# Kernel tuning notes

Measured on AMD Instinct MI355X. Metric: run time of the kernel, lower is better.

The kernel has to match this reference:

```python
import jax, jax.numpy as jnp
import numpy as np

N_NODES = 10000
N_EDGES = 320000
D = 256


def setup_inputs() -> dict:
    key = jax.random.key(0)
    k_x, k_w, k_m, k_s, k_d = jax.random.split(key, 5)
    x = jax.random.normal(k_x, (N_NODES, D), dtype=jnp.float32)
    W = jax.random.normal(k_w, (D, D), dtype=jnp.float32)
    M = jax.random.normal(k_m, (D, D), dtype=jnp.float32)
    edge_src = jax.random.randint(k_s, (N_EDGES,), 0, N_NODES, dtype=jnp.int64)
    edge_dst = jax.random.randint(k_d, (N_EDGES,), 0, N_NODES, dtype=jnp.int64)
    return {"x": x, "W": W, "M": M, "edge_src": edge_src, "edge_dst": edge_dst}


def reference(x, W, M, edge_src, edge_dst):
    # Synchronous GCN-style update: new_x_i = relu(x_i @ W + sum_{j in N(i)} x_j @ M)
    # Transform once [N,d]@[d,d], then gather per-edge and segment-sum into destinations.
    self_term = x @ W                      # [N, d]
    msg = x @ M                            # [N, d]
    agg = jax.ops.segment_sum(msg[edge_src], edge_dst, num_segments=x.shape[0])  # [N, d]
    return jax.nn.relu(self_term + agg)
```

## Files before the change

kernel.cpp:

```cpp
#include <hip/hip_runtime.h>
#include <hip/hip_bf16.h>
#include <stdint.h>

#define N_NODES 10000
#define N_EDGES 320000
#define DD 256
#define BKT 96

typedef __attribute__((ext_vector_type(4))) float f32x4;
typedef __attribute__((ext_vector_type(8))) short short8;
typedef __attribute__((ext_vector_type(4))) short short4v;

__device__ __forceinline__ short f2b(float f) {
  unsigned u = __builtin_bit_cast(unsigned, f);
  u += 0x7fffu + ((u >> 16) & 1u);
  return (short)(u >> 16);
}
__device__ __forceinline__ float b2f(short s) {
  return __builtin_bit_cast(float, ((unsigned)(unsigned short)s) << 16);
}

__global__ __launch_bounds__(256) void k_pre(const float* __restrict__ x,
                                             const float* __restrict__ W,
                                             const float* __restrict__ M,
                                             const int* __restrict__ esrc,
                                             const int* __restrict__ edst,
                                             short* __restrict__ xb,
                                             short* __restrict__ Bb,
                                             int* __restrict__ cnt,
                                             int* __restrict__ srcs) {
  const int b = blockIdx.x, t = threadIdx.x;
  if (b < 2500) {
    int i = (b * 256 + t) * 4;
    f32x4 v = *(const f32x4*)(x + i);
    short4v o;
    o[0] = f2b(v[0]); o[1] = f2b(v[1]); o[2] = f2b(v[2]); o[3] = f2b(v[3]);
    *(short4v*)(xb + i) = o;
  } else if (b < 2756) {
    int n = b - 2500;
    Bb[n * 512 + t]       = f2b(W[t * DD + n]);
    Bb[n * 512 + t + 256] = f2b(M[t * DD + n]);
  } else {
    int e = (b - 2756) * 256 + t;
    int d = edst[e];
    int pos = atomicAdd(&cnt[d], 1);
    if (pos < BKT) srcs[d * BKT + pos] = esrc[e];
  }
}

__global__ __launch_bounds__(256) void k_agg(const short* __restrict__ xb,
                                             const int* __restrict__ cnt,
                                             const int* __restrict__ srcs,
                                             short* __restrict__ axb) {
  const int wave = threadIdx.x >> 6, lane = threadIdx.x & 63;
  const int node = blockIdx.x * 4 + wave;
  const int col = lane * 4;
  const int* bkt = srcs + node * BKT;
  float a0 = 0.f, a1 = 0.f, a2 = 0.f, a3 = 0.f;
  const int d = cnt[node];
  int e = 0;
  for (; e + 16 <= d; e += 16) {
    int sidx[16];
    #pragma unroll
    for (int q = 0; q < 16; q++) sidx[q] = bkt[e + q];
    short4v vv[16];
    #pragma unroll
    for (int q = 0; q < 16; q++) vv[q] = *(const short4v*)(xb + sidx[q] * DD + col);
    #pragma unroll
    for (int q = 0; q < 16; q++) {
      a0 += b2f(vv[q][0]); a1 += b2f(vv[q][1]);
      a2 += b2f(vv[q][2]); a3 += b2f(vv[q][3]);
    }
  }
  for (; e < d; e++) {
    int s = bkt[e];
    short4v v = *(const short4v*)(xb + s * DD + col);
    a0 += b2f(v[0]); a1 += b2f(v[1]); a2 += b2f(v[2]); a3 += b2f(v[3]);
  }
  short4v o;
  o[0] = f2b(a0); o[1] = f2b(a1); o[2] = f2b(a2); o[3] = f2b(a3);
  *(short4v*)(axb + node * DD + col) = o;
}

__global__ __launch_bounds__(256) void k_gemm(const short* __restrict__ xb,
                                              const short* __restrict__ axb,
                                              const short* __restrict__ Bb,
                                              float* __restrict__ out) {
  __shared__ short Bs[32 * 520];
  const int tid = threadIdx.x;
  const int wave = tid >> 6, lane = tid & 63;
  const int m0 = blockIdx.x * 64, n0 = blockIdx.y * 64;
  const int wr = (wave >> 1) * 32, wc = (wave & 1) * 32;
  const int lr = lane & 15, lkb = (lane >> 4) * 8;

  int ar0 = m0 + wr + lr;       if (ar0 > N_NODES - 1) ar0 = N_NODES - 1;
  int ar1 = m0 + wr + 16 + lr;  if (ar1 > N_NODES - 1) ar1 = N_NODES - 1;

  const int R0 = wc + lr, R1 = wc + 16 + lr;
  const int bb0 = (R0 >> 1) * 520 + (R0 & 1) * 256 + lkb;
  const int bb1 = (R1 >> 1) * 520 + (R1 & 1) * 256 + lkb;

  f32x4 acc[2][2] = {};

  #pragma unroll
  for (int h = 0; h < 2; h++) {
    const short* __restrict__ Asrc = h ? axb : xb;
    for (int c = wave; c < 32; c += 4) {
      const short* src = Bb + (n0 + 2 * c + (lane >> 5)) * 512 + h * 256 + (lane & 31) * 8;
      __builtin_amdgcn_global_load_lds(
          (const __attribute__((address_space(1))) unsigned int*)src,
          (__attribute__((address_space(3))) unsigned int*)(&Bs[c * 520]),
          16, 0, 0);
    }
    __syncthreads();
    #pragma unroll
    for (int kk = 0; kk < 256; kk += 32) {
      short8 a0 = *(const short8*)(Asrc + ar0 * DD + kk + lkb);
      short8 a1 = *(const short8*)(Asrc + ar1 * DD + kk + lkb);
      short8 b0 = *(const short8*)(&Bs[bb0 + kk]);
      short8 b1 = *(const short8*)(&Bs[bb1 + kk]);
      acc[0][0] = __builtin_amdgcn_mfma_f32_16x16x32_bf16(a0, b0, acc[0][0], 0, 0, 0);
      acc[0][1] = __builtin_amdgcn_mfma_f32_16x16x32_bf16(a0, b1, acc[0][1], 0, 0, 0);
      acc[1][0] = __builtin_amdgcn_mfma_f32_16x16x32_bf16(a1, b0, acc[1][0], 0, 0, 0);
      acc[1][1] = __builtin_amdgcn_mfma_f32_16x16x32_bf16(a1, b1, acc[1][1], 0, 0, 0);
    }
    __syncthreads();
  }

  const int rb = (lane >> 4) * 4, cb = lane & 15;
  #pragma unroll
  for (int i = 0; i < 2; i++) {
    #pragma unroll
    for (int r = 0; r < 4; r++) {
      int gm = m0 + wr + i * 16 + rb + r;
      if (gm < N_NODES) {
        int go = gm * DD + n0 + wc + cb;
        out[go]      = fmaxf(acc[i][0][r], 0.f);
        out[go + 16] = fmaxf(acc[i][1][r], 0.f);
      }
    }
  }
}

extern "C" void kernel_launch(void* const* d_in, const int* in_sizes, int n_in,
                              void* d_out, int out_size, void* d_ws, size_t ws_size,
                              hipStream_t stream) {
  const float* x = (const float*)d_in[0];
  const float* W = (const float*)d_in[1];
  const float* M = (const float*)d_in[2];
  const int* esrc = (const int*)d_in[3];
  const int* edst = (const int*)d_in[4];
  float* out = (float*)d_out;

  char* w = (char*)d_ws;
  short* xb  = (short*)w;
  short* axb = (short*)(w + 5120000);
  short* Bb  = (short*)(w + 10240000);
  int* cnt   = (int*)(w + 10502144);
  int* srcs  = cnt + N_NODES;

  hipMemsetAsync(cnt, 0, N_NODES * sizeof(int), stream);
  k_pre<<<4006, 256, 0, stream>>>(x, W, M, esrc, edst, xb, Bb, cnt, srcs);
  k_agg<<<2500, 256, 0, stream>>>(xb, cnt, srcs, axb);
  k_gemm<<<dim3(157, 4), 256, 0, stream>>>(xb, axb, Bb, out);
}
```

Before: 133.6 us.

## Use 16-byte gathers with two nodes per wave and a zero-pad row in aggregation

The aggregation kernel now assigns two destination nodes per wave, 32 lanes each, and every lane loads 8 bf16 values (16 bytes) per neighbour instead of 4. Neighbour counts are padded up to the pair's maximum in steps of 16, and missing slots read a zeroed pad row so the loop needs no scalar tail. This aims at wider memory transactions and better latency hiding per gather. The preprocessing kernel also reorders its block ranges so the atomic bucketing blocks are scheduled first, and the memset now also clears the pad row. The cost is wasted loads when the two paired nodes have different degrees.

```diff
diff --git a/kernel.cpp b/kernel.cpp
--- a/kernel.cpp
+++ b/kernel.cpp
@@ -30,56 +30,65 @@
                                              int* __restrict__ cnt,
                                              int* __restrict__ srcs) {
   const int b = blockIdx.x, t = threadIdx.x;
-  if (b < 2500) {
-    int i = (b * 256 + t) * 4;
+  if (b < 1250) {
+    int e = b * 256 + t;
+    int d = edst[e];
+    int pos = atomicAdd(&cnt[d], 1);
+    if (pos < BKT) srcs[d * BKT + pos] = esrc[e];
+  } else if (b < 3750) {
+    int i = ((b - 1250) * 256 + t) * 4;
     f32x4 v = *(const f32x4*)(x + i);
     short4v o;
     o[0] = f2b(v[0]); o[1] = f2b(v[1]); o[2] = f2b(v[2]); o[3] = f2b(v[3]);
     *(short4v*)(xb + i) = o;
-  } else if (b < 2756) {
-    int n = b - 2500;
+  } else {
+    int n = b - 3750;
     Bb[n * 512 + t]       = f2b(W[t * DD + n]);
     Bb[n * 512 + t + 256] = f2b(M[t * DD + n]);
-  } else {
-    int e = (b - 2756) * 256 + t;
-    int d = edst[e];
-    int pos = atomicAdd(&cnt[d], 1);
-    if (pos < BKT) srcs[d * BKT + pos] = esrc[e];
   }
 }
 
 __global__ __launch_bounds__(256) void k_agg(const short* __restrict__ xb,
+                                             const short* __restrict__ zpad,
                                              const int* __restrict__ cnt,
                                              const int* __restrict__ srcs,
                                              short* __restrict__ axb) {
   const int wave = threadIdx.x >> 6, lane = threadIdx.x & 63;
-  const int node = blockIdx.x * 4 + wave;
-  const int col = lane * 4;
+  const int half = lane >> 5, sl = lane & 31;
+  const int node = (blockIdx.x * 4 + wave) * 2 + half;
+  const int col = sl * 8;
   const int* bkt = srcs + node * BKT;
-  float a0 = 0.f, a1 = 0.f, a2 = 0.f, a3 = 0.f;
-  const int d = cnt[node];
-  int e = 0;
-  for (; e + 16 <= d; e += 16) {
+  int d = cnt[node];
+  if (d > BKT) d = BKT;
+  int dmax = d;
+  { int o = __shfl_xor(dmax, 32); dmax = dmax > o ? dmax : o; }
+
+  float a0=0.f,a1=0.f,a2=0.f,a3=0.f,a4=0.f,a5=0.f,a6=0.f,a7=0.f;
+  for (int e = 0; e < dmax; e += 16) {
     int sidx[16];
     #pragma unroll
-    for (int q = 0; q < 16; q++) sidx[q] = bkt[e + q];
-    short4v vv[16];
+    for (int q = 0; q < 16; q++) {
+      int idx = e + q;
+      sidx[q] = bkt[idx < d ? idx : 0];
+    }
+    short8 vv[16];
     #pragma unroll
-    for (int q = 0; q < 16; q++) vv[q] = *(const short4v*)(xb + sidx[q] * DD + col);
+    for (int q = 0; q < 16; q++) {
+      const short* p = ((e + q) < d) ? (xb + sidx[q] * DD) : zpad;
+      vv[q] = *(const short8*)(p + col);
+    }
     #pragma unroll
     for (int q = 0; q < 16; q++) {
       a0 += b2f(vv[q][0]); a1 += b2f(vv[q][1]);
       a2 += b2f(vv[q][2]); a3 += b2f(vv[q][3]);
+      a4 += b2f(vv[q][4]); a5 += b2f(vv[q][5]);
+      a6 += b2f(vv[q][6]); a7 += b2f(vv[q][7]);
     }
   }
-  for (; e < d; e++) {
-    int s = bkt[e];
-    short4v v = *(const short4v*)(xb + s * DD + col);
-    a0 += b2f(v[0]); a1 += b2f(v[1]); a2 += b2f(v[2]); a3 += b2f(v[3]);
-  }
-  short4v o;
+  short8 o;
   o[0] = f2b(a0); o[1] = f2b(a1); o[2] = f2b(a2); o[3] = f2b(a3);
-  *(short4v*)(axb + node * DD + col) = o;
+  o[4] = f2b(a4); o[5] = f2b(a5); o[6] = f2b(a6); o[7] = f2b(a7);
+  *(short8*)(axb + node * DD + col) = o;
 }
 
 __global__ __launch_bounds__(256) void k_gemm(const short* __restrict__ xb,
@@ -153,14 +162,15 @@
   float* out = (float*)d_out;
 
   char* w = (char*)d_ws;
-  short* xb  = (short*)w;
-  short* axb = (short*)(w + 5120000);
-  short* Bb  = (short*)(w + 10240000);
-  int* cnt   = (int*)(w + 10502144);
-  int* srcs  = cnt + N_NODES;
+  short* xb   = (short*)w;
+  short* axb  = (short*)(w + 5120000);
+  short* Bb   = (short*)(w + 10240000);
+  int*   cnt  = (int*)(w + 10502144);
+  short* zpad = (short*)(w + 10542144);
+  int*   srcs = (int*)(w + 10542656);
 
-  hipMemsetAsync(cnt, 0, N_NODES * sizeof(int), stream);
+  hipMemsetAsync(cnt, 0, 40512, stream);
   k_pre<<<4006, 256, 0, stream>>>(x, W, M, esrc, edst, xb, Bb, cnt, srcs);
-  k_agg<<<2500, 256, 0, stream>>>(xb, cnt, srcs, axb);
+  k_agg<<<1250, 256, 0, stream>>>(xb, zpad, cnt, srcs, axb);
   k_gemm<<<dim3(157, 4), 256, 0, stream>>>(xb, axb, Bb, out);
 }
```

New measurement: 127.9 us. -4.2%, faster.
